# Performance work log

Hardware: AMD Instinct MI355X
Metric: run time of the kernel (lower is better)

Reference implementation:

```python
import jax, jax.numpy as jnp
import numpy as np
import math

E = 8        # num_experts
L2 = 15
L3 = 32
D = 3072     # eval_features_per_perspective
R = 256      # router_features
B = 16384
AUX_ALPHA = 0.01
Z_ALPHA = 0.001


def setup_inputs() -> dict:
    key = jax.random.key(0)
    ks = jax.random.split(key, 12)
    inp = {
        "expert_input": jax.random.uniform(ks[0], (B, D), jnp.float32),
        "router_input": jax.random.normal(ks[1], (R,) , jnp.float32) * 0 + jax.random.normal(ks[1], (B, R), jnp.float32),
        # router init: normal(std=0.01), zero bias (as in _reset_router)
        "router_w": jax.random.normal(ks[2], (E, R), jnp.float32) * 0.01,
        "router_b": jnp.zeros((E,), jnp.float32),
        # FactorizedStackedLinear l1: stacked weight [E*(L2+1), D] + shared factorized [(L2+1), D]
        "l1_w": jax.random.normal(ks[3], (E * (L2 + 1), D), jnp.float32) * (1.0 / math.sqrt(D)),
        "l1_b": jax.random.normal(ks[4], (E * (L2 + 1),), jnp.float32) * 0.01,
        "l1f_w": jax.random.normal(ks[5], (L2 + 1, D), jnp.float32) * (1.0 / math.sqrt(D)),
        "l1f_b": jax.random.normal(ks[6], (L2 + 1,), jnp.float32) * 0.01,
        # StackedLinear l2: [E*L3, 2*L2]
        "l2_w": jax.random.normal(ks[7], (E * L3, 2 * L2), jnp.float32) * (1.0 / math.sqrt(2 * L2)),
        "l2_b": jax.random.normal(ks[8], (E * L3,), jnp.float32) * 0.01,
        # StackedLinear output: [E*1, L3], bias zeroed in __init__
        "out_w": jax.random.normal(ks[9], (E, L3), jnp.float32) * (1.0 / math.sqrt(L3)),
        "out_b": jnp.zeros((E,), jnp.float32),
    }
    return inp


def reference(expert_input, router_input, router_w, router_b,
              l1_w, l1_b, l1f_w, l1f_b, l2_w, l2_b, out_w, out_b):
    # ---- router + straight-through hard gate ----
    gate_logits = router_input @ router_w.T + router_b                      # [B, E]
    gate_probs = jax.nn.softmax(gate_logits, axis=-1)
    expert_indices = jnp.argmax(gate_logits, axis=-1)                       # [B]
    hard_gate = jax.nn.one_hot(expert_indices, E, dtype=gate_probs.dtype)   # [B, E]
    gate = hard_gate + gate_probs - jax.lax.stop_gradient(gate_probs)

    # ---- routing metrics / losses ----
    fraction_routed = hard_gate.mean(axis=0)                                 # [E]
    avg_gate_prob = gate_probs.mean(axis=0)                                  # [E]
    aux_loss = E * jnp.sum(fraction_routed * avg_gate_prob)
    z_loss = jnp.mean(jnp.square(jax.nn.logsumexp(gate_logits, axis=-1)))
    entropy = jnp.mean(-jnp.sum(gate_probs * jnp.log(jnp.clip(gate_probs, 1e-9)), axis=-1))
    normalized_entropy = entropy / jnp.float32(math.log(max(E, 2)))
    top1_prob = jnp.mean(jnp.max(gate_probs, axis=-1))
    router_loss = jnp.float32(AUX_ALPHA) * aux_loss + jnp.float32(Z_ALPHA) * z_loss  # training path

    # ---- l1: FactorizedStackedLinear, dense over all experts (training path) ----
    merged_w = (l1_w + jnp.tile(l1f_w, (E, 1))).reshape(E, L2 + 1, D)        # [E, L2+1, D]
    merged_b = (l1_b + jnp.tile(l1f_b, (E,))).reshape(E, L2 + 1)             # [E, L2+1]
    l1c = jnp.einsum('bi,eoi->beo', expert_input, merged_w) + merged_b[None]  # [B, E, L2+1]
    l1x, l1x_out = l1c[:, :, :L2], l1c[:, :, L2:]                            # [B,E,L2], [B,E,1]
    l1x = jnp.clip(jnp.concatenate([jnp.square(l1x) * (255.0 / 256.0), l1x], axis=2), 0.0, 1.0)  # [B,E,2*L2]

    # ---- l2 + output StackedLinear ----
    w2 = l2_w.reshape(E, L3, 2 * L2)
    l2x = jnp.clip(jnp.einsum('bei,eoi->beo', l1x, w2) + l2_b.reshape(E, L3)[None], 0.0, 1.0)  # [B,E,L3]
    wo = out_w.reshape(E, 1, L3)
    l3x = jnp.einsum('bei,eoi->beo', l2x, wo) + out_b.reshape(E, 1)[None] + l1x_out            # [B,E,1]

    # ---- gated combine ----
    out = jnp.einsum('be,beo->bo', gate, l3x)                                # [B, 1]
    return (out, router_loss, aux_loss, z_loss, fraction_routed, avg_gate_prob,
            normalized_entropy, top1_prob)
```

## Files before the change

### kernel.cpp

```cpp
#include <hip/hip_runtime.h>

constexpr int NB  = 16384;
constexpr int ND  = 3072;
constexpr int NR  = 256;
constexpr int NE  = 8;
constexpr int NO1 = 16;
constexpr int NL2D = 30;
constexpr int NL3 = 32;

constexpr size_t WS_CURSORS = 32;
constexpr size_t WS_OFFPAD  = 128;
constexpr size_t WS_IDX     = 256;
constexpr size_t WS_BUCKET  = WS_IDX + (size_t)NB*4;
constexpr size_t WS_MB      = WS_BUCKET + (size_t)(NB+256)*4;
constexpr size_t WS_MW      = WS_MB + 512;
constexpr size_t WS_BLK_CNT  = WS_MW + (size_t)128*3072*4;
constexpr size_t WS_BLK_SUMP = WS_BLK_CNT + 8192;
constexpr size_t WS_BLK_Z    = WS_BLK_SUMP + 8192;
constexpr size_t WS_BLK_ENT  = WS_BLK_Z + 1024;
constexpr size_t WS_BLK_TOP  = WS_BLK_ENT + 1024;

__device__ __forceinline__ float clamp01(float v) { return fminf(fmaxf(v, 0.0f), 1.0f); }

__global__ __launch_bounds__(256) void router_merge_kernel(
    const float* __restrict__ rin, const float* __restrict__ rw,
    const float* __restrict__ rb, int* __restrict__ idx,
    int* __restrict__ blk_cnt, float* __restrict__ blk_sump,
    float* __restrict__ blk_z, float* __restrict__ blk_ent, float* __restrict__ blk_top,
    const float* __restrict__ l1w, const float* __restrict__ l1b,
    const float* __restrict__ l1fw, const float* __restrict__ l1fb,
    float* __restrict__ mw, float* __restrict__ mb)
{
    const int t = threadIdx.x;

    if (blockIdx.x >= 256) {
        const int gid = blockIdx.x - 256;
        const int i4 = gid * 256 + t;
        const float4 a = ((const float4*)l1w)[i4];
        const float4 b = ((const float4*)l1fw)[i4 % (NO1 * ND / 4)];
        float4 r; r.x = a.x + b.x; r.y = a.y + b.y; r.z = a.z + b.z; r.w = a.w + b.w;
        ((float4*)mw)[i4] = r;
        if (gid == 0 && t < NE * NO1) {
            mb[t] = l1b[t] + l1fb[t & (NO1 - 1)];
        }
        return;
    }

    __shared__ float w_s[NE][NR];
    __shared__ float red_f[4][11];
    __shared__ int   red_c[4][8];

    {
        const float4* src = (const float4*)rw;
        float4* dst = (float4*)&w_s[0][0];
        dst[t]       = src[t];
        dst[t + 256] = src[t + 256];
    }
    __syncthreads();

    const int q  = t & 3;
    const int rr = t >> 2;
    const int b  = blockIdx.x * 64 + rr;
    const float* rp = rin + (size_t)b * NR + q * 64;

    float acc[NE];
#pragma unroll
    for (int e = 0; e < NE; ++e) acc[e] = 0.0f;

#pragma unroll
    for (int c = 0; c < 16; ++c) {
        const float4 xv = *(const float4*)(rp + c * 4);
#pragma unroll
        for (int e = 0; e < NE; ++e) {
            const float4 wv = *(const float4*)(&w_s[e][q * 64 + c * 4]);
            acc[e] = fmaf(xv.x, wv.x, acc[e]);
            acc[e] = fmaf(xv.y, wv.y, acc[e]);
            acc[e] = fmaf(xv.z, wv.z, acc[e]);
            acc[e] = fmaf(xv.w, wv.w, acc[e]);
        }
    }
    float lg[NE];
#pragma unroll
    for (int e = 0; e < NE; ++e) {
        float v = acc[e];
        v += __shfl_xor(v, 1);
        v += __shfl_xor(v, 2);
        lg[e] = v + rb[e];
    }

    float m = lg[0]; int am = 0;
#pragma unroll
    for (int e = 1; e < NE; ++e) { if (lg[e] > m) { m = lg[e]; am = e; } }
    float p[NE]; float ssum = 0.0f;
#pragma unroll
    for (int e = 0; e < NE; ++e) { p[e] = __expf(lg[e] - m); ssum += p[e]; }
    const float inv = 1.0f / ssum;
    const float lse = m + __logf(ssum);

    const bool active = (q == 0);
    float sv[11];
    float ent = 0.0f, top = 0.0f;
#pragma unroll
    for (int e = 0; e < NE; ++e) {
        const float pj = p[e] * inv;
        sv[e] = pj;
        ent -= pj * __logf(fmaxf(pj, 1e-9f));
        top = fmaxf(top, pj);
    }
    sv[8] = lse * lse;
    sv[9] = ent;
    sv[10] = top;
    if (!active) {
#pragma unroll
        for (int i = 0; i < 11; ++i) sv[i] = 0.0f;
    }
    if (active) idx[b] = am;

#pragma unroll
    for (int i = 0; i < 11; ++i) {
        float v = sv[i];
        v += __shfl_xor(v, 4);
        v += __shfl_xor(v, 8);
        v += __shfl_xor(v, 16);
        v += __shfl_xor(v, 32);
        sv[i] = v;
    }
    int cnt[NE];
#pragma unroll
    for (int j = 0; j < NE; ++j) {
        unsigned long long mk = __ballot(active && (am == j));
        cnt[j] = __popcll(mk);
    }

    const int wave = t >> 6;
    if ((t & 63) == 0) {
#pragma unroll
        for (int i = 0; i < 11; ++i) red_f[wave][i] = sv[i];
#pragma unroll
        for (int j = 0; j < NE; ++j) red_c[wave][j] = cnt[j];
    }
    __syncthreads();

    const int bid = blockIdx.x;
    if (t < 8) {
        blk_sump[bid * 8 + t] = red_f[0][t] + red_f[1][t] + red_f[2][t] + red_f[3][t];
        blk_cnt [bid * 8 + t] = red_c[0][t] + red_c[1][t] + red_c[2][t] + red_c[3][t];
    } else if (t == 8) {
        blk_z[bid]   = red_f[0][8] + red_f[1][8] + red_f[2][8] + red_f[3][8];
    } else if (t == 9) {
        blk_ent[bid] = red_f[0][9] + red_f[1][9] + red_f[2][9] + red_f[3][9];
    } else if (t == 10) {
        blk_top[bid] = red_f[0][10] + red_f[1][10] + red_f[2][10] + red_f[3][10];
    }
}

__global__ __launch_bounds__(256) void scatter_finalize_kernel(
    const int* __restrict__ blk_cnt, const float* __restrict__ blk_sump,
    const float* __restrict__ blk_z, const float* __restrict__ blk_ent,
    const float* __restrict__ blk_top, const int* __restrict__ idx,
    int* __restrict__ cursors, int* __restrict__ bucket,
    int* __restrict__ offpad, float* __restrict__ out)
{
    const int t = threadIdx.x;

    if (blockIdx.x == 64) {
        __shared__ float ps_s[32][8];
        __shared__ int   pc_s[32][8];
        __shared__ float zet_s[3][4];
        __shared__ float tot_f[8];
        __shared__ int   tot_c[8];
        {
            const int e = t & 7, g = t >> 3;
            float ps = 0.0f; int pc = 0;
#pragma unroll
            for (int k = 0; k < 8; ++k) {
                const int bb = g * 8 + k;
                ps += blk_sump[bb * 8 + e];
                pc += blk_cnt [bb * 8 + e];
            }
            ps_s[g][e] = ps;
            pc_s[g][e] = pc;
        }
        {
            float z = blk_z[t], en = blk_ent[t], tp = blk_top[t];
#pragma unroll
            for (int o = 1; o < 64; o <<= 1) {
                z  += __shfl_xor(z, o);
                en += __shfl_xor(en, o);
                tp += __shfl_xor(tp, o);
            }
            const int wave = t >> 6;
            if ((t & 63) == 0) { zet_s[0][wave] = z; zet_s[1][wave] = en; zet_s[2][wave] = tp; }
        }
        __syncthreads();
        if (t < 8) {
            float s = 0.0f; int c = 0;
            for (int g = 0; g < 32; ++g) { s += ps_s[g][t]; c += pc_s[g][t]; }
            tot_f[t] = s; tot_c[t] = c;
        }
        __syncthreads();
        if (t == 0) {
            int run = 0;
#pragma unroll
            for (int e = 0; e < NE; ++e) {
                offpad[e] = run;
                run += (tot_c[e] + 31) & ~31;
            }
            offpad[NE] = run;

            const float invB = 1.0f / (float)NB;
            float aux = 0.0f;
            float frac[NE], avg[NE];
#pragma unroll
            for (int e = 0; e < NE; ++e) {
                frac[e] = (float)tot_c[e] * invB;
                avg[e]  = tot_f[e] * invB;
                aux += frac[e] * avg[e];
            }
            aux *= (float)NE;
            const float z   = (zet_s[0][0] + zet_s[0][1] + zet_s[0][2] + zet_s[0][3]) * invB;
            const float ent = (zet_s[1][0] + zet_s[1][1] + zet_s[1][2] + zet_s[1][3]) * invB;
            const float top = (zet_s[2][0] + zet_s[2][1] + zet_s[2][2] + zet_s[2][3]) * invB;
            const float rl  = 0.01f * aux + 0.001f * z;

            float* o = out + NB;
            o[0] = rl;
            o[1] = aux;
            o[2] = z;
#pragma unroll
            for (int e = 0; e < NE; ++e) o[3 + e]  = frac[e];
#pragma unroll
            for (int e = 0; e < NE; ++e) o[11 + e] = avg[e];
            o[19] = ent / __logf(8.0f);
            o[20] = top;
        }
        return;
    }

    __shared__ int red_c[4][8];
    __shared__ int offp[8];
    {
        const int4 a = ((const int4*)blk_cnt)[t * 2];
        const int4 bql = ((const int4*)blk_cnt)[t * 2 + 1];
        int v[8] = {a.x, a.y, a.z, a.w, bql.x, bql.y, bql.z, bql.w};
#pragma unroll
        for (int j = 0; j < 8; ++j) {
#pragma unroll
            for (int o = 1; o < 64; o <<= 1) v[j] += __shfl_xor(v[j], o);
        }
        const int wave = t >> 6;
        if ((t & 63) == 0) {
#pragma unroll
            for (int j = 0; j < 8; ++j) red_c[wave][j] = v[j];
        }
    }
    __syncthreads();
    if (t == 0) {
        int run = 0;
#pragma unroll
        for (int e = 0; e < NE; ++e) {
            offp[e] = run;
            run += (red_c[0][e] + red_c[1][e] + red_c[2][e] + red_c[3][e] + 31) & ~31;
        }
    }
    __syncthreads();

    const int b = blockIdx.x * 256 + t;
    const int e = idx[b];
    const int lane = t & 63;
#pragma unroll
    for (int ee = 0; ee < NE; ++ee) {
        unsigned long long mask = __ballot(e == ee);
        if (e == ee) {
            int leader = __ffsll((unsigned long long)mask) - 1;
            int cnt = __popcll(mask);
            int base = 0;
            if (lane == leader) base = atomicAdd(&cursors[ee], cnt);
            base = __shfl(base, leader);
            int pos = base + __popcll(mask & ((1ull << lane) - 1ull));
            bucket[offp[ee] + pos] = b;
        }
    }
}

__global__ __launch_bounds__(256) void moe_main_kernel(
    const float* __restrict__ x, const float* __restrict__ mw,
    const float* __restrict__ mb, const float* __restrict__ l2w,
    const float* __restrict__ l2b, const float* __restrict__ ow,
    const float* __restrict__ ob, const int* __restrict__ bucket,
    const int* __restrict__ offpad, float* __restrict__ out)
{
    __shared__ int   rows_s[16];
    __shared__ int   expert_s;
    __shared__ float l1c_s[16][16];
    __shared__ float l1x_s[16][30];
    __shared__ float l1c15_s[16];

    const int t = threadIdx.x;
    const int slot0 = blockIdx.x * 16;
    if (t < 16) rows_s[t] = bucket[slot0 + t];
    if (t == 0) {
        int e = 0;
#pragma unroll
        for (int j = 1; j < NE; ++j) if (slot0 >= offpad[j]) e = j;
        expert_s = e;
    }
    __syncthreads();

    const int e    = expert_s;
    const int wid  = t >> 6;
    const int lane = t & 63;

    const float* xsrc[4];
#pragma unroll
    for (int rr = 0; rr < 4; ++rr) {
        int r = rows_s[4 * wid + rr];
        if (r < 0) r = 0;
        xsrc[rr] = x + (size_t)r * ND + lane * 4;
    }
    const float* wbase = mw + (size_t)e * NO1 * ND + lane * 4;

    float acc[4][16];
#pragma unroll
    for (int rr = 0; rr < 4; ++rr)
#pragma unroll
        for (int o = 0; o < 16; ++o) acc[rr][o] = 0.0f;

    float4 xcur[4], xnxt[4];
#pragma unroll
    for (int rr = 0; rr < 4; ++rr) xcur[rr] = *(const float4*)(xsrc[rr]);
#pragma unroll
    for (int rr = 0; rr < 4; ++rr) xnxt[rr] = xcur[rr];

    for (int c = 0; c < 12; ++c) {
        if (c + 1 < 12) {
#pragma unroll
            for (int rr = 0; rr < 4; ++rr)
                xnxt[rr] = *(const float4*)(xsrc[rr] + (c + 1) * 256);
        }

        const float* wk = wbase + c * 256;
#pragma unroll
        for (int o = 0; o < 16; ++o) {
            const float4 wv = *(const float4*)(wk + (size_t)o * ND);
#pragma unroll
            for (int rr = 0; rr < 4; ++rr) {
                float a = acc[rr][o];
                a = fmaf(xcur[rr].x, wv.x, a);
                a = fmaf(xcur[rr].y, wv.y, a);
                a = fmaf(xcur[rr].z, wv.z, a);
                a = fmaf(xcur[rr].w, wv.w, a);
                acc[rr][o] = a;
            }
        }
#pragma unroll
        for (int rr = 0; rr < 4; ++rr) xcur[rr] = xnxt[rr];
    }

#pragma unroll
    for (int rr = 0; rr < 4; ++rr)
#pragma unroll
        for (int o = 0; o < 16; ++o) {
            float a = acc[rr][o];
            a += __shfl_xor(a, 1);
            a += __shfl_xor(a, 2);
            a += __shfl_xor(a, 4);
            a += __shfl_xor(a, 8);
            a += __shfl_xor(a, 16);
            a += __shfl_xor(a, 32);
            acc[rr][o] = a;
        }
    if (lane == 0) {
#pragma unroll
        for (int rr = 0; rr < 4; ++rr)
#pragma unroll
            for (int o = 0; o < 16; ++o)
                l1c_s[4 * wid + rr][o] = acc[rr][o];
    }
    __syncthreads();

    const int r = t >> 4;
    const int q = t & 15;
    const int rowb = rows_s[r];

    {
        const int o = q;
        float v = l1c_s[r][o] + mb[e * NO1 + o];
        if (o < 15) {
            l1x_s[r][o]      = clamp01(v * v * (255.0f / 256.0f));
            l1x_s[r][o + 15] = clamp01(v);
        } else {
            l1c15_s[r] = v;
        }
    }
    __syncthreads();

    float pacc = 0.0f;
#pragma unroll
    for (int oo = 0; oo < 2; ++oo) {
        const int o2 = q + oo * 16;
        float a2 = l2b[e * NL3 + o2];
        const float* w2r = l2w + (size_t)e * NL3 * NL2D + o2 * NL2D;
#pragma unroll
        for (int i = 0; i < NL2D; ++i) a2 = fmaf(l1x_s[r][i], w2r[i], a2);
        a2 = clamp01(a2);
        pacc = fmaf(a2, ow[e * NL3 + o2], pacc);
    }
    pacc += __shfl_xor(pacc, 1);
    pacc += __shfl_xor(pacc, 2);
    pacc += __shfl_xor(pacc, 4);
    pacc += __shfl_xor(pacc, 8);

    if (q == 0 && rowb >= 0) {
        out[rowb] = pacc + ob[e] + l1c15_s[r];
    }
}

extern "C" void kernel_launch(void* const* d_in, const int* in_sizes, int n_in,
                              void* d_out, int out_size, void* d_ws, size_t ws_size,
                              hipStream_t stream)
{
    const float* x    = (const float*)d_in[0];
    const float* rin  = (const float*)d_in[1];
    const float* rw   = (const float*)d_in[2];
    const float* rb   = (const float*)d_in[3];
    const float* l1w  = (const float*)d_in[4];
    const float* l1b  = (const float*)d_in[5];
    const float* l1fw = (const float*)d_in[6];
    const float* l1fb = (const float*)d_in[7];
    const float* l2w  = (const float*)d_in[8];
    const float* l2b  = (const float*)d_in[9];
    const float* ow   = (const float*)d_in[10];
    const float* ob   = (const float*)d_in[11];
    float* out = (float*)d_out;

    char* ws = (char*)d_ws;
    int*   cursors = (int*)(ws + WS_CURSORS);
    int*   offpad  = (int*)(ws + WS_OFFPAD);
    int*   idx     = (int*)(ws + WS_IDX);
    int*   bucket  = (int*)(ws + WS_BUCKET);
    float* mb      = (float*)(ws + WS_MB);
    float* mw      = (float*)(ws + WS_MW);
    int*   blk_cnt  = (int*)(ws + WS_BLK_CNT);
    float* blk_sump = (float*)(ws + WS_BLK_SUMP);
    float* blk_z    = (float*)(ws + WS_BLK_Z);
    float* blk_ent  = (float*)(ws + WS_BLK_ENT);
    float* blk_top  = (float*)(ws + WS_BLK_TOP);

    hipMemsetAsync(ws, 0, 256, stream);
    hipMemsetAsync(ws + WS_BUCKET, 0xFF, (size_t)(NB + 256) * 4, stream);

    router_merge_kernel<<<640, 256, 0, stream>>>(rin, rw, rb, idx, blk_cnt, blk_sump,
                                                 blk_z, blk_ent, blk_top,
                                                 l1w, l1b, l1fw, l1fb, mw, mb);
    scatter_finalize_kernel<<<65, 256, 0, stream>>>(blk_cnt, blk_sump, blk_z, blk_ent,
                                                    blk_top, idx, cursors, bucket,
                                                    offpad, out);
    moe_main_kernel<<<(NB + 256) / 16, 256, 0, stream>>>(x, mw, mb, l2w, l2b, ow, ob,
                                                         bucket, offpad, out);
}
```

Baseline: 113.1 us.

## Stage expert-input rows in LDS via async global_load_lds, split outputs across waves

The main MoE kernel now copies each 16-row tile of expert input into a double-buffered LDS tile with the async global-to-LDS load builtin. Each wave computes 4 of the 16 l1 outputs for all 16 rows, instead of all 16 outputs for 4 rows. This cuts the per-wave merged-weight reads from 16 rows to 4 and lets all waves share the staged activations. In exchange it adds a block-wide barrier per chunk and 32KB of LDS per block, which may lower occupancy. The per-row shuffle reductions stay the same in total count.

After: 114.1 us. About the same (+0.9%).

```diff
diff --git a/kernel.cpp b/kernel.cpp
--- a/kernel.cpp
+++ b/kernel.cpp
@@ -22,6 +22,13 @@
 
 __device__ __forceinline__ float clamp01(float v) { return fminf(fmaxf(v, 0.0f), 1.0f); }
 
+__device__ __forceinline__ void stage16(const float* g, float* l) {
+    __builtin_amdgcn_global_load_lds(
+        (const __attribute__((address_space(1))) unsigned int*)g,
+        (__attribute__((address_space(3))) unsigned int*)l,
+        16, 0, 0);
+}
+
 __global__ __launch_bounds__(256) void router_merge_kernel(
     const float* __restrict__ rin, const float* __restrict__ rw,
     const float* __restrict__ rb, int* __restrict__ idx,
@@ -290,6 +297,7 @@
     const float* __restrict__ ob, const int* __restrict__ bucket,
     const int* __restrict__ offpad, float* __restrict__ out)
 {
+    __shared__ float x_lds[2][16][256];
     __shared__ int   rows_s[16];
     __shared__ int   expert_s;
     __shared__ float l1c_s[16][16];
@@ -318,64 +326,70 @@
         if (r < 0) r = 0;
         xsrc[rr] = x + (size_t)r * ND + lane * 4;
     }
-    const float* wbase = mw + (size_t)e * NO1 * ND + lane * 4;
-
-    float acc[4][16];
+    const float* wbase = mw + (size_t)e * NO1 * ND + (size_t)(4 * wid) * ND + lane * 4;
+
+    float acc[16][4];
+#pragma unroll
+    for (int rr = 0; rr < 16; ++rr)
+#pragma unroll
+        for (int oo = 0; oo < 4; ++oo) acc[rr][oo] = 0.0f;
+
 #pragma unroll
     for (int rr = 0; rr < 4; ++rr)
-#pragma unroll
-        for (int o = 0; o < 16; ++o) acc[rr][o] = 0.0f;
-
-    float4 xcur[4], xnxt[4];
-#pragma unroll
-    for (int rr = 0; rr < 4; ++rr) xcur[rr] = *(const float4*)(xsrc[rr]);
-#pragma unroll
-    for (int rr = 0; rr < 4; ++rr) xnxt[rr] = xcur[rr];
+        stage16(xsrc[rr], &x_lds[0][4 * wid + rr][0]);
+    __syncthreads();
 
     for (int c = 0; c < 12; ++c) {
+        const int cur = c & 1;
+        const int nxt = cur ^ 1;
         if (c + 1 < 12) {
+            const int off = (c + 1) * 256;
 #pragma unroll
             for (int rr = 0; rr < 4; ++rr)
-                xnxt[rr] = *(const float4*)(xsrc[rr] + (c + 1) * 256);
+                stage16(xsrc[rr] + off, &x_lds[nxt][4 * wid + rr][0]);
         }
 
         const float* wk = wbase + c * 256;
-#pragma unroll
-        for (int o = 0; o < 16; ++o) {
-            const float4 wv = *(const float4*)(wk + (size_t)o * ND);
-#pragma unroll
-            for (int rr = 0; rr < 4; ++rr) {
-                float a = acc[rr][o];
-                a = fmaf(xcur[rr].x, wv.x, a);
-                a = fmaf(xcur[rr].y, wv.y, a);
-                a = fmaf(xcur[rr].z, wv.z, a);
-                a = fmaf(xcur[rr].w, wv.w, a);
-                acc[rr][o] = a;
+        float4 wv[4];
+#pragma unroll
+        for (int oo = 0; oo < 4; ++oo)
+            wv[oo] = *(const float4*)(wk + (size_t)oo * ND);
+
+#pragma unroll
+        for (int rr = 0; rr < 16; ++rr) {
+            const float4 xv = *(const float4*)&x_lds[cur][rr][lane * 4];
+#pragma unroll
+            for (int oo = 0; oo < 4; ++oo) {
+                float a = acc[rr][oo];
+                a = fmaf(xv.x, wv[oo].x, a);
+                a = fmaf(xv.y, wv[oo].y, a);
+                a = fmaf(xv.z, wv[oo].z, a);
+                a = fmaf(xv.w, wv[oo].w, a);
+                acc[rr][oo] = a;
             }
         }
-#pragma unroll
-        for (int rr = 0; rr < 4; ++rr) xcur[rr] = xnxt[rr];
-    }
-
-#pragma unroll
-    for (int rr = 0; rr < 4; ++rr)
-#pragma unroll
-        for (int o = 0; o < 16; ++o) {
-            float a = acc[rr][o];
+        __syncthreads();
+    }
+
+#pragma unroll
+    for (int rr = 0; rr < 16; ++rr)
+#pragma unroll
+        for (int oo = 0; oo < 4; ++oo) {
+            float a = acc[rr][oo];
             a += __shfl_xor(a, 1);
             a += __shfl_xor(a, 2);
             a += __shfl_xor(a, 4);
             a += __shfl_xor(a, 8);
             a += __shfl_xor(a, 16);
             a += __shfl_xor(a, 32);
-            acc[rr][o] = a;
+            acc[rr][oo] = a;
         }
     if (lane == 0) {
 #pragma unroll
-        for (int rr = 0; rr < 4; ++rr)
-#pragma unroll
-            for (int o = 0; o < 16; ++o)
-                l1c_s[4 * wid + rr][o] = acc[rr][o];
+        for (int rr = 0; rr < 16; ++rr)
+#pragma unroll
+            for (int oo = 0; oo < 4; ++oo)
+                l1c_s[rr][4 * wid + oo] = acc[rr][oo];
     }
     __syncthreads();
 
```
